# Kernel optimization log

Hardware: AMD Instinct MI355X
Metric: run time of the kernel (lower is better)

The kernel has to match this reference:

```python
import jax, jax.numpy as jnp
import numpy as np

N_NODES = 50000
N_EDGES = 1_600_000
N_REL = 8
D_IN = 128
D_OUT = 128


def _unique_edges(rng, n_nodes, n_rel, n_edges):
    # Torch module clamps the dense adjacency to 0/1, so duplicate
    # (rel, src, dst) triples collapse; generate unique edges so the
    # edge-list formulation matches exactly.
    m = 2 * n_edges
    src = rng.integers(0, n_nodes, m)
    dst = rng.integers(0, n_nodes, m)
    et = rng.integers(0, n_rel, m)
    key = (et.astype(np.int64) * n_nodes + src) * n_nodes + dst
    _, idx = np.unique(key, return_index=True)
    idx = np.sort(idx)[:n_edges]
    return src[idx], dst[idx], et[idx]


def setup_inputs() -> dict:
    key = jax.random.key(0)
    kx, kw, kr, kb = jax.random.split(key, 4)
    rng = np.random.default_rng(0)
    src, dst, et = _unique_edges(rng, N_NODES, N_REL, N_EDGES)
    bound = 1.0 / np.sqrt(D_OUT)
    return {
        "x": jax.random.normal(kx, (N_NODES, D_IN), dtype=jnp.float32),
        "edge_index": jnp.asarray(np.stack([src, dst]), dtype=jnp.int64),
        "edge_type": jnp.asarray(et, dtype=jnp.int64),
        "weight": jax.random.uniform(kw, (N_REL, D_OUT, D_IN), minval=-bound, maxval=bound, dtype=jnp.float32),
        "root": jax.random.uniform(kr, (D_OUT, D_IN), minval=-bound, maxval=bound, dtype=jnp.float32),
        "bias": jax.random.uniform(kb, (D_OUT,), minval=-bound, maxval=bound, dtype=jnp.float32),
    }


def reference(x, edge_index, edge_type, weight, root, bias):
    # Math identical to: adj[l, src, dst] = 1; adj row-normalized (mean);
    # out = sum_r norm_adj_r @ x @ W_r^T + x @ root^T + bias.
    n_rel, d_out, d_in = weight.shape
    n_nodes = x.shape[0]
    src = edge_index[0]
    dst = edge_index[1]
    seg = (edge_type * n_nodes + src).astype(jnp.int32)  # segment per (rel, node)
    num_seg = n_rel * n_nodes
    # sum of neighbor features per (relation, node): [R*N, d_in]
    agg = jax.ops.segment_sum(x[dst], seg, num_segments=num_seg)
    deg = jax.ops.segment_sum(jnp.ones((src.shape[0],), dtype=x.dtype), seg, num_segments=num_seg)
    norm = jnp.where(deg > 0, 1.0 / deg, 0.0)[:, None]  # mean aggr, nan_to_num(0)
    agg = (agg * norm).reshape(n_rel, n_nodes, d_in)
    out = jnp.einsum('rnd,rod->no', agg, weight)
    out = out + x @ root.T + bias[None]
    return out
```

## Files before the change

### kernel.cpp

```cpp
#include <hip/hip_runtime.h>


#define D 128
#define SCAN_CHUNK 2048
#define SEG_BITS 9
#define SEGS_PER_BUCKET 512
#define NBLK 128

typedef __attribute__((ext_vector_type(8))) short short8;
typedef __attribute__((ext_vector_type(4))) float v4f;
typedef __attribute__((ext_vector_type(4))) unsigned uint4v;

#define GLOAD_LDS16(gptr, lptr) \
    __builtin_amdgcn_global_load_lds((const __attribute__((address_space(1))) void*)(gptr), \
                                     (__attribute__((address_space(3))) void*)(lptr), 16, 0, 0)

__device__ __forceinline__ unsigned short f2b(float f) {
    union { float f; unsigned u; } v; v.f = f;
    unsigned r = v.u + 0x7fffu + ((v.u >> 16) & 1u);
    return (unsigned short)(r >> 16);
}
__device__ __forceinline__ float blo(unsigned u) {
    union { unsigned u; float f; } v; v.u = u << 16; return v.f;
}
__device__ __forceinline__ float bhi(unsigned u) {
    union { unsigned u; float f; } v; v.u = u & 0xffff0000u; return v.f;
}

__global__ void cvt_bf16_all(const float* __restrict__ x, long long nx,
                             const float* __restrict__ w, long long nw,
                             const float* __restrict__ root, long long nr,
                             unsigned short* __restrict__ xB,
                             unsigned short* __restrict__ xRow,
                             unsigned short* __restrict__ wB, int nN) {
    long long i = ((long long)blockIdx.x * blockDim.x + threadIdx.x) * 4;
    if (i < nx) {
        float4 v = *(const float4*)(x + i);
        uint2 p;
        p.x = (unsigned)f2b(v.x) | ((unsigned)f2b(v.y) << 16);
        p.y = (unsigned)f2b(v.z) | ((unsigned)f2b(v.w) << 16);
        long long n = i >> 7;
        int d = (int)(i & 127);
        size_t o = (size_t)(d >> 5) * (size_t)nN * 32 + (size_t)n * 32 + (d & 31);
        *(uint2*)(xB + o) = p;
        *(uint2*)(xRow + i) = p;
        return;
    }
    const float* src;
    unsigned short* dst;
    long long j;
    if (i < nx + nw) { src = w; dst = wB; j = i - nx; }
    else if (i < nx + nw + nr) { src = root; dst = wB + nw; j = i - nx - nw; }
    else return;
    float4 v = *(const float4*)(src + j);
    uint2 p;
    p.x = (unsigned)f2b(v.x) | ((unsigned)f2b(v.y) << 16);
    p.y = (unsigned)f2b(v.z) | ((unsigned)f2b(v.w) << 16);
    *(uint2*)(dst + j) = p;
}

__global__ __launch_bounds__(256)
void histA(const int* __restrict__ ei, const int* __restrict__ et,
           int* __restrict__ blockHist, int nE, int nN, int B, int epb) {
    __shared__ int lh[1024];
    const int tid = threadIdx.x;
    for (int b = tid; b < B; b += 256) lh[b] = 0;
    __syncthreads();
    const int base = blockIdx.x * epb;
    const int lim = min(base + epb, nE);
    for (int e = base + tid; e < lim; e += 256) {
        int seg = et[e] * nN + ei[e];
        atomicAdd(&lh[seg >> SEG_BITS], 1);
    }
    __syncthreads();
    for (int b = tid; b < B; b += 256)
        blockHist[b * NBLK + blockIdx.x] = lh[b];
}

__global__ __launch_bounds__(256)
void scan1(const int* __restrict__ in, int* __restrict__ excl,
           int* __restrict__ blockSums, int n) {
    __shared__ int t[256];
    const int tid = threadIdx.x;
    const int base = blockIdx.x * SCAN_CHUNK + tid * 8;
    int v[8];
    int tot = 0;
#pragma unroll
    for (int i = 0; i < 8; i++) {
        v[i] = (base + i < n) ? in[base + i] : 0;
        tot += v[i];
    }
    t[tid] = tot;
    __syncthreads();
    for (int off = 1; off < 256; off <<= 1) {
        int add = (tid >= off) ? t[tid - off] : 0;
        __syncthreads();
        t[tid] += add;
        __syncthreads();
    }
    int run = t[tid] - tot;
#pragma unroll
    for (int i = 0; i < 8; i++) {
        if (base + i < n) excl[base + i] = run;
        run += v[i];
    }
    if (tid == 255) blockSums[blockIdx.x] = t[255];
}

__global__ __launch_bounds__(256)
void scan2(int* __restrict__ blockSums, int nb) {
    __shared__ int t[256];
    const int tid = threadIdx.x;
    int v = (tid < nb) ? blockSums[tid] : 0;
    t[tid] = v;
    __syncthreads();
    for (int off = 1; off < 256; off <<= 1) {
        int add = (tid >= off) ? t[tid - off] : 0;
        __syncthreads();
        t[tid] += add;
        __syncthreads();
    }
    if (tid < nb) blockSums[tid] = t[tid] - v;
}

__global__ __launch_bounds__(256)
void scan3s(int* __restrict__ excl, const int* __restrict__ blockSums, int n) {
    const int base = blockIdx.x * SCAN_CHUNK + threadIdx.x * 8;
    const int bs = blockSums[blockIdx.x];
#pragma unroll
    for (int i = 0; i < 8; i++)
        if (base + i < n) excl[base + i] += bs;
}

__global__ __launch_bounds__(256)
void scatterA(const int* __restrict__ ei, const int* __restrict__ et,
              const int* __restrict__ scanned, unsigned* __restrict__ bucketEdges,
              int nE, int nN, int B, int epb) {
    __shared__ int cur[1024];
    const int tid = threadIdx.x;
    for (int b = tid; b < B; b += 256) cur[b] = scanned[b * NBLK + blockIdx.x];
    __syncthreads();
    const int base = blockIdx.x * epb;
    const int lim = min(base + epb, nE);
    for (int e = base + tid; e < lim; e += 256) {
        int seg = et[e] * nN + ei[e];
        int bkt = seg >> SEG_BITS;
        unsigned pk = ((unsigned)(seg & (SEGS_PER_BUCKET - 1)) << 16) | (unsigned)ei[nE + e];
        int pos = atomicAdd(&cur[bkt], 1);
        bucketEdges[pos] = pk;
    }
}

__global__ __launch_bounds__(256)
void segOff(const unsigned* __restrict__ bucketEdges, const int* __restrict__ scanned,
            int* __restrict__ off, unsigned short* __restrict__ sortedDst,
            int nE, int numSeg, int B) {
    __shared__ int lh[SEGS_PER_BUCKET];
    __shared__ int sc[256];
    __shared__ int lcur[SEGS_PER_BUCKET];
    const int tid = threadIdx.x;
    const int b = blockIdx.x;
    const int eBase = scanned[b * NBLK];
    const int eEnd = (b + 1 < B) ? scanned[(b + 1) * NBLK] : nE;
    const int segBase = b * SEGS_PER_BUCKET;
    const int segLim = min(SEGS_PER_BUCKET, numSeg - segBase);

    lh[2 * tid] = 0; lh[2 * tid + 1] = 0;
    __syncthreads();
    for (int i = eBase + tid; i < eEnd; i += 256)
        atomicAdd(&lh[bucketEdges[i] >> 16], 1);
    __syncthreads();
    int a0 = lh[2 * tid], a1 = lh[2 * tid + 1];
    sc[tid] = a0 + a1;
    __syncthreads();
    for (int o = 1; o < 256; o <<= 1) {
        int add = (tid >= o) ? sc[tid - o] : 0;
        __syncthreads();
        sc[tid] += add;
        __syncthreads();
    }
    int pairBase = sc[tid] - (a0 + a1);
    int g0 = eBase + pairBase;
    int g1 = g0 + a0;
    lcur[2 * tid] = g0;
    lcur[2 * tid + 1] = g1;
    if (2 * tid < segLim)     off[segBase + 2 * tid] = g0;
    if (2 * tid + 1 < segLim) off[segBase + 2 * tid + 1] = g1;
    if (b == B - 1 && tid == 0) off[numSeg] = nE;
    __syncthreads();
    for (int i = eBase + tid; i < eEnd; i += 256) {
        unsigned u = bucketEdges[i];
        int pos = atomicAdd(&lcur[u >> 16], 1);
        sortedDst[pos] = (unsigned short)(u & 0xFFFFu);
    }
}

__global__ __launch_bounds__(256)
void rgcn_gather(const unsigned short* __restrict__ xB,
                 const unsigned short* __restrict__ sortedDst,
                 const int* __restrict__ off,
                 unsigned short* __restrict__ Abuf, int nN, size_t SL) {
    const int tid = threadIdx.x;
    const int lane = tid & 63;
    const int idx4 = lane & 3;
    const int grp = lane >> 2;
    const int wv = tid >> 6;
    const int n = blockIdx.x * 64 + wv * 16 + grp;
    const int r = blockIdx.y;
    const int sl = blockIdx.z;
    const bool valid = (n < nN);
    const int seg = valid ? (r * nN + n) : 0;

    const int start = off[seg];
    int cnt = valid ? (off[seg + 1] - start) : 0;

    int mx = cnt;
    mx = max(mx, __shfl_xor(mx, 4));
    mx = max(mx, __shfl_xor(mx, 8));
    mx = max(mx, __shfl_xor(mx, 16));
    mx = max(mx, __shfl_xor(mx, 32));

    float2 acc2[4];
#pragma unroll
    for (int i = 0; i < 4; i++) acc2[i] = make_float2(0.f, 0.f);

    const unsigned short* xSlab = xB + (size_t)sl * nN * 32 + idx4 * 8;

    for (int b = 0; b < mx; b += 4) {
        int myDst = (b + idx4 < cnt) ? (int)sortedDst[start + b + idx4] : 0;
        uint4v v[4];
#pragma unroll
        for (int j = 0; j < 4; j++) {
            int dst = __shfl(myDst, grp * 4 + j);
            bool act = (b + j < cnt);
            v[j] = act ? *(const uint4v*)(xSlab + ((size_t)dst << 5))
                       : (uint4v){0u, 0u, 0u, 0u};
        }
#pragma unroll
        for (int j = 0; j < 4; j++) {
            acc2[0].x += blo(v[j].x); acc2[0].y += bhi(v[j].x);
            acc2[1].x += blo(v[j].y); acc2[1].y += bhi(v[j].y);
            acc2[2].x += blo(v[j].z); acc2[2].y += bhi(v[j].z);
            acc2[3].x += blo(v[j].w); acc2[3].y += bhi(v[j].w);
        }
    }

    if (valid) {
        float s = cnt > 0 ? 1.0f / (float)cnt : 0.f;
        uint4v pkt;
        pkt.x = (unsigned)f2b(acc2[0].x * s) | ((unsigned)f2b(acc2[0].y * s) << 16);
        pkt.y = (unsigned)f2b(acc2[1].x * s) | ((unsigned)f2b(acc2[1].y * s) << 16);
        pkt.z = (unsigned)f2b(acc2[2].x * s) | ((unsigned)f2b(acc2[2].y * s) << 16);
        pkt.w = (unsigned)f2b(acc2[3].x * s) | ((unsigned)f2b(acc2[3].y * s) << 16);
        __builtin_nontemporal_store(pkt,
            (uint4v*)(Abuf + (size_t)r * SL + (size_t)n * D + sl * 32 + idx4 * 8));
    }
}

__global__ __launch_bounds__(256)
void rgcn_gemm_mfma(const unsigned short* __restrict__ A,
                    const unsigned short* __restrict__ wB,
                    const float* __restrict__ bias,
                    float* __restrict__ out, int nN, int nRel, size_t SL) {
    __shared__ __align__(16) unsigned short As[2][64 * 64];
    __shared__ __align__(16) unsigned short Bs[2][128 * 64];
    const int tid = threadIdx.x;
    const int wave = tid >> 6;
    const int lane = tid & 63;
    const int wm = wave & 1;
    const int wn = wave >> 1;
    const int m16 = lane & 15;
    const int q = lane >> 4;
    const int row0 = blockIdx.x * 64;

    v4f acc[2][4];
#pragma unroll
    for (int i = 0; i < 2; i++)
#pragma unroll
        for (int j = 0; j < 4; j++) acc[i][j] = (v4f){0.f, 0.f, 0.f, 0.f};

    const int sw = m16 & 7;
    int aoff[2][2], boff[4][2];
#pragma unroll
    for (int mt = 0; mt < 2; mt++) {
        int row = wm * 32 + mt * 16 + m16;
#pragma unroll
        for (int kb = 0; kb < 2; kb++)
            aoff[mt][kb] = row * 64 + (((kb * 4 + q) ^ sw) * 8);
    }
#pragma unroll
    for (int nt = 0; nt < 4; nt++) {
        int o = wn * 64 + nt * 16 + m16;
#pragma unroll
        for (int kb = 0; kb < 2; kb++)
            boff[nt][kb] = o * 64 + (((kb * 4 + q) ^ sw) * 8);
    }

    const int l8 = lane >> 3;
    const int gd = (lane & 7) ^ l8;
    const size_t aBase = (size_t)(row0 + wave * 16 + l8) * D + gd * 8;
    const size_t bBase = (size_t)(wave * 32 + l8) * D + gd * 8;

    const int nT = 2 * (nRel + 1);

#define STAGE(buf, t) do { \
        const int s_ = (t) >> 1, h_ = (t) & 1; \
        const unsigned short* ga_ = A + (size_t)s_ * SL + h_ * 64 + aBase; \
        const unsigned short* gb_ = wB + (size_t)s_ * (D * D) + h_ * 64 + bBase; \
        GLOAD_LDS16(ga_,        &As[buf][(wave * 2 + 0) * 512]); \
        GLOAD_LDS16(ga_ + 1024, &As[buf][(wave * 2 + 1) * 512]); \
        GLOAD_LDS16(gb_,        &Bs[buf][(wave * 4 + 0) * 512]); \
        GLOAD_LDS16(gb_ + 1024, &Bs[buf][(wave * 4 + 1) * 512]); \
        GLOAD_LDS16(gb_ + 2048, &Bs[buf][(wave * 4 + 2) * 512]); \
        GLOAD_LDS16(gb_ + 3072, &Bs[buf][(wave * 4 + 3) * 512]); \
    } while (0)

    STAGE(0, 0);
    __syncthreads();
    int cur = 0;
    for (int t = 0; t < nT; ++t) {
        if (t + 1 < nT) STAGE(cur ^ 1, t + 1);
        const unsigned short* Ab = As[cur];
        const unsigned short* Bb = Bs[cur];
        short8 a[2][2], b[4][2];
#pragma unroll
        for (int kb = 0; kb < 2; kb++) {
#pragma unroll
            for (int mt = 0; mt < 2; mt++)
                a[mt][kb] = *(const short8*)&Ab[aoff[mt][kb]];
#pragma unroll
            for (int nt = 0; nt < 4; nt++)
                b[nt][kb] = *(const short8*)&Bb[boff[nt][kb]];
        }
#pragma unroll
        for (int kb = 0; kb < 2; kb++)
#pragma unroll
            for (int mt = 0; mt < 2; mt++)
#pragma unroll
                for (int nt = 0; nt < 4; nt++)
                    acc[mt][nt] = __builtin_amdgcn_mfma_f32_16x16x32_bf16(
                        a[mt][kb], b[nt][kb], acc[mt][nt], 0, 0, 0);
        __syncthreads();
        cur ^= 1;
    }
#undef STAGE

#pragma unroll
    for (int mt = 0; mt < 2; mt++) {
#pragma unroll
        for (int nt = 0; nt < 4; nt++) {
            int col = wn * 64 + nt * 16 + m16;
            float bi = bias[col];
#pragma unroll
            for (int reg = 0; reg < 4; reg++) {
                int rrow = row0 + wm * 32 + mt * 16 + q * 4 + reg;
                if (rrow < nN)
                    out[(size_t)rrow * D + col] = acc[mt][nt][reg] + bi;
            }
        }
    }
}

extern "C" void kernel_launch(void* const* d_in, const int* in_sizes, int n_in,
                              void* d_out, int out_size, void* d_ws, size_t ws_size,
                              hipStream_t stream) {
    const float* x    = (const float*)d_in[0];
    const int*   ei   = (const int*)d_in[1];
    const int*   et   = (const int*)d_in[2];
    const float* w    = (const float*)d_in[3];
    const float* root = (const float*)d_in[4];
    const float* bias = (const float*)d_in[5];
    float* out = (float*)d_out;

    const int nN   = in_sizes[0] / D;
    const int nE   = in_sizes[2];
    const int nRel = in_sizes[3] / (D * D);
    const int numSeg = nRel * nN;
    const int B = (numSeg + SEGS_PER_BUCKET - 1) >> SEG_BITS;
    const int nBH = B * NBLK;
    const int epb = (nE + NBLK - 1) / NBLK;
    const int nNalloc = (nN + 63) & ~63;
    const size_t SL = (size_t)nNalloc * D;

    char* p = (char*)d_ws;
    unsigned* bucketEdges   = (unsigned*)p;        p += (size_t)nE * sizeof(unsigned);
    unsigned short* sortedDst = (unsigned short*)p; p += (size_t)nE * sizeof(unsigned short);
    p = (char*)(((uintptr_t)p + 255) & ~(uintptr_t)255);
    int* off       = (int*)p;  p += (size_t)(numSeg + 1) * sizeof(int);
    int* blockHist = (int*)p;  p += (size_t)nBH * sizeof(int);
    int* scanned   = (int*)p;  p += (size_t)nBH * sizeof(int);
    int* blockSums = (int*)p;  p += 256 * sizeof(int);
    p = (char*)(((uintptr_t)p + 255) & ~(uintptr_t)255);
    unsigned short* xB   = (unsigned short*)p;  p += (size_t)nN * D * sizeof(unsigned short);
    unsigned short* wBc  = (unsigned short*)p;  p += (size_t)(nRel + 1) * D * D * sizeof(unsigned short);
    p = (char*)(((uintptr_t)p + 255) & ~(uintptr_t)255);
    unsigned short* Abuf = (unsigned short*)p;
    unsigned short* xRow = Abuf + (size_t)nRel * SL;

    const int nScanBlocks = (nBH + SCAN_CHUNK - 1) / SCAN_CHUNK;

    histA<<<NBLK, 256, 0, stream>>>(ei, et, blockHist, nE, nN, B, epb);
    scan1<<<nScanBlocks, 256, 0, stream>>>(blockHist, scanned, blockSums, nBH);
    scan2<<<1, 256, 0, stream>>>(blockSums, nScanBlocks);
    scan3s<<<nScanBlocks, 256, 0, stream>>>(scanned, blockSums, nBH);
    scatterA<<<NBLK, 256, 0, stream>>>(ei, et, scanned, bucketEdges, nE, nN, B, epb);
    segOff<<<B, 256, 0, stream>>>(bucketEdges, scanned, off, sortedDst, nE, numSeg, B);

    long long nx = (long long)nN * D;
    long long nw = (long long)nRel * D * D;
    long long nr = (long long)D * D;
    long long ncvt = (nx + nw + nr) / 4;
    cvt_bf16_all<<<(int)((ncvt + 255) / 256), 256, 0, stream>>>(x, nx, w, nw, root, nr,
                                                                xB, xRow, wBc, nN);

    dim3 gg((nN + 63) / 64, nRel, 4);
    rgcn_gather<<<gg, 256, 0, stream>>>(xB, sortedDst, off, Abuf, nN, SL);

    rgcn_gemm_mfma<<<(nN + 63) / 64, 256, 0, stream>>>(Abuf, wBc, bias, out, nN, nRel, SL);
}
```

Measured before the change: 278.4 us.

## Sort segments by degree for balanced gather and fold scan fixup into consumers

Builds a degree histogram in segOff and a permutation of segments grouped by degree (a counting sort), so each gather wavefront processes segments with similar neighbor counts and loses less time to divergence from the per-wave max loop. It also removes the scan3s kernel by adding blockSums when scatterA and segOff read offsets, and uses packed f32 adds in the accumulation. The cost is an extra permBuild kernel, a perm indirection, and scattered output writes in the gather.

```diff
diff --git a/kernel.cpp b/kernel.cpp
--- a/kernel.cpp
+++ b/kernel.cpp
@@ -6,9 +6,11 @@
 #define SEG_BITS 9
 #define SEGS_PER_BUCKET 512
 #define NBLK 128
+#define NDEG 32
 
 typedef __attribute__((ext_vector_type(8))) short short8;
 typedef __attribute__((ext_vector_type(4))) float v4f;
+typedef __attribute__((ext_vector_type(2))) float f32x2;
 typedef __attribute__((ext_vector_type(4))) unsigned uint4v;
 
 #define GLOAD_LDS16(gptr, lptr) \
@@ -79,7 +81,12 @@
 
 __global__ __launch_bounds__(256)
 void scan1(const int* __restrict__ in, int* __restrict__ excl,
-           int* __restrict__ blockSums, int n) {
+           int* __restrict__ blockSums, int* __restrict__ degHist,
+           int* __restrict__ cursor32, int n) {
+    if (blockIdx.x == 0 && threadIdx.x < 2 * NDEG) {
+        if (threadIdx.x < NDEG) degHist[threadIdx.x] = 0;
+        else cursor32[threadIdx.x - NDEG] = 0;
+    }
     __shared__ int t[256];
     const int tid = threadIdx.x;
     const int base = blockIdx.x * SCAN_CHUNK + tid * 8;
@@ -124,21 +131,16 @@
 }
 
 __global__ __launch_bounds__(256)
-void scan3s(int* __restrict__ excl, const int* __restrict__ blockSums, int n) {
-    const int base = blockIdx.x * SCAN_CHUNK + threadIdx.x * 8;
-    const int bs = blockSums[blockIdx.x];
-#pragma unroll
-    for (int i = 0; i < 8; i++)
-        if (base + i < n) excl[base + i] += bs;
-}
-
-__global__ __launch_bounds__(256)
 void scatterA(const int* __restrict__ ei, const int* __restrict__ et,
-              const int* __restrict__ scanned, unsigned* __restrict__ bucketEdges,
+              const int* __restrict__ scanned, const int* __restrict__ blockSums,
+              unsigned* __restrict__ bucketEdges,
               int nE, int nN, int B, int epb) {
     __shared__ int cur[1024];
     const int tid = threadIdx.x;
-    for (int b = tid; b < B; b += 256) cur[b] = scanned[b * NBLK + blockIdx.x];
+    for (int b = tid; b < B; b += 256) {
+        int idx = b * NBLK + blockIdx.x;
+        cur[b] = scanned[idx] + blockSums[idx >> 11];
+    }
     __syncthreads();
     const int base = blockIdx.x * epb;
     const int lim = min(base + epb, nE);
@@ -153,24 +155,34 @@
 
 __global__ __launch_bounds__(256)
 void segOff(const unsigned* __restrict__ bucketEdges, const int* __restrict__ scanned,
+            const int* __restrict__ blockSums,
             int* __restrict__ off, unsigned short* __restrict__ sortedDst,
-            int nE, int numSeg, int B) {
+            int* __restrict__ degHist, int nE, int numSeg, int B) {
     __shared__ int lh[SEGS_PER_BUCKET];
     __shared__ int sc[256];
     __shared__ int lcur[SEGS_PER_BUCKET];
+    __shared__ int dh[NDEG];
     const int tid = threadIdx.x;
     const int b = blockIdx.x;
-    const int eBase = scanned[b * NBLK];
-    const int eEnd = (b + 1 < B) ? scanned[(b + 1) * NBLK] : nE;
+    const int i0 = b * NBLK;
+    const int eBase = scanned[i0] + blockSums[i0 >> 11];
+    int eEnd = nE;
+    if (b + 1 < B) {
+        const int i1 = (b + 1) * NBLK;
+        eEnd = scanned[i1] + blockSums[i1 >> 11];
+    }
     const int segBase = b * SEGS_PER_BUCKET;
     const int segLim = min(SEGS_PER_BUCKET, numSeg - segBase);
 
     lh[2 * tid] = 0; lh[2 * tid + 1] = 0;
+    if (tid < NDEG) dh[tid] = 0;
     __syncthreads();
     for (int i = eBase + tid; i < eEnd; i += 256)
         atomicAdd(&lh[bucketEdges[i] >> 16], 1);
     __syncthreads();
     int a0 = lh[2 * tid], a1 = lh[2 * tid + 1];
+    if (2 * tid < segLim)     atomicAdd(&dh[min(a0, NDEG - 1)], 1);
+    if (2 * tid + 1 < segLim) atomicAdd(&dh[min(a1, NDEG - 1)], 1);
     sc[tid] = a0 + a1;
     __syncthreads();
     for (int o = 1; o < 256; o <<= 1) {
@@ -193,23 +205,59 @@
         int pos = atomicAdd(&lcur[u >> 16], 1);
         sortedDst[pos] = (unsigned short)(u & 0xFFFFu);
     }
+    __syncthreads();
+    if (tid < NDEG && dh[tid]) atomicAdd(&degHist[tid], dh[tid]);
+}
+
+__global__ __launch_bounds__(256)
+void permBuild(const int* __restrict__ off, const int* __restrict__ degHist,
+               int* __restrict__ cursor32, int* __restrict__ perm, int numSeg) {
+    __shared__ int lcnt[NDEG];
+    __shared__ int lbase[NDEG];
+    __shared__ int gbase[NDEG];
+    const int tid = threadIdx.x;
+    if (tid < NDEG) lcnt[tid] = 0;
+    __syncthreads();
+    int s[4], bkt[4], lpos[4];
+#pragma unroll
+    for (int i = 0; i < 4; i++) {
+        s[i] = blockIdx.x * 1024 + i * 256 + tid;
+        bkt[i] = -1;
+        if (s[i] < numSeg) {
+            int c = off[s[i] + 1] - off[s[i]];
+            bkt[i] = min(c, NDEG - 1);
+            lpos[i] = atomicAdd(&lcnt[bkt[i]], 1);
+        }
+    }
+    __syncthreads();
+    if (tid < NDEG) {
+        lbase[tid] = lcnt[tid] ? atomicAdd(&cursor32[tid], lcnt[tid]) : 0;
+        int run = 0;
+        for (int k = 0; k < tid; k++) run += degHist[k];
+        gbase[tid] = run;
+    }
+    __syncthreads();
+#pragma unroll
+    for (int i = 0; i < 4; i++)
+        if (bkt[i] >= 0)
+            perm[gbase[bkt[i]] + lbase[bkt[i]] + lpos[i]] = s[i];
 }
 
 __global__ __launch_bounds__(256)
 void rgcn_gather(const unsigned short* __restrict__ xB,
                  const unsigned short* __restrict__ sortedDst,
-                 const int* __restrict__ off,
-                 unsigned short* __restrict__ Abuf, int nN, size_t SL) {
+                 const int* __restrict__ off, const int* __restrict__ perm,
+                 unsigned short* __restrict__ Abuf, int nN, int numSeg,
+                 size_t SL, unsigned long long M) {
     const int tid = threadIdx.x;
     const int lane = tid & 63;
     const int idx4 = lane & 3;
     const int grp = lane >> 2;
     const int wv = tid >> 6;
-    const int n = blockIdx.x * 64 + wv * 16 + grp;
-    const int r = blockIdx.y;
-    const int sl = blockIdx.z;
-    const bool valid = (n < nN);
-    const int seg = valid ? (r * nN + n) : 0;
+    const int gsi = blockIdx.x * 64 + wv * 16 + grp;
+    const int sl = blockIdx.y;
+    const bool valid = (gsi < numSeg);
+    const int seg = valid ? perm[gsi] : 0;
 
     const int start = off[seg];
     int cnt = valid ? (off[seg + 1] - start) : 0;
@@ -220,9 +268,9 @@
     mx = max(mx, __shfl_xor(mx, 16));
     mx = max(mx, __shfl_xor(mx, 32));
 
-    float2 acc2[4];
-#pragma unroll
-    for (int i = 0; i < 4; i++) acc2[i] = make_float2(0.f, 0.f);
+    f32x2 acc2[4];
+#pragma unroll
+    for (int i = 0; i < 4; i++) acc2[i] = (f32x2){0.f, 0.f};
 
     const unsigned short* xSlab = xB + (size_t)sl * nN * 32 + idx4 * 8;
 
@@ -238,14 +286,20 @@
         }
 #pragma unroll
         for (int j = 0; j < 4; j++) {
-            acc2[0].x += blo(v[j].x); acc2[0].y += bhi(v[j].x);
-            acc2[1].x += blo(v[j].y); acc2[1].y += bhi(v[j].y);
-            acc2[2].x += blo(v[j].z); acc2[2].y += bhi(v[j].z);
-            acc2[3].x += blo(v[j].w); acc2[3].y += bhi(v[j].w);
+            f32x2 t0 = (f32x2){blo(v[j].x), bhi(v[j].x)};
+            f32x2 t1 = (f32x2){blo(v[j].y), bhi(v[j].y)};
+            f32x2 t2 = (f32x2){blo(v[j].z), bhi(v[j].z)};
+            f32x2 t3 = (f32x2){blo(v[j].w), bhi(v[j].w)};
+            asm("v_pk_add_f32 %0, %0, %1" : "+v"(acc2[0]) : "v"(t0));
+            asm("v_pk_add_f32 %0, %0, %1" : "+v"(acc2[1]) : "v"(t1));
+            asm("v_pk_add_f32 %0, %0, %1" : "+v"(acc2[2]) : "v"(t2));
+            asm("v_pk_add_f32 %0, %0, %1" : "+v"(acc2[3]) : "v"(t3));
         }
     }
 
     if (valid) {
+        const int r = (int)(((unsigned long long)seg * M) >> 48);
+        const int n = seg - r * nN;
         float s = cnt > 0 ? 1.0f / (float)cnt : 0.f;
         uint4v pkt;
         pkt.x = (unsigned)f2b(acc2[0].x * s) | ((unsigned)f2b(acc2[0].y * s) << 16);
@@ -381,6 +435,7 @@
     const int epb = (nE + NBLK - 1) / NBLK;
     const int nNalloc = (nN + 63) & ~63;
     const size_t SL = (size_t)nNalloc * D;
+    const unsigned long long M = ((1ULL << 48) + nN - 1) / nN;
 
     char* p = (char*)d_ws;
     unsigned* bucketEdges   = (unsigned*)p;        p += (size_t)nE * sizeof(unsigned);
@@ -390,6 +445,10 @@
     int* blockHist = (int*)p;  p += (size_t)nBH * sizeof(int);
     int* scanned   = (int*)p;  p += (size_t)nBH * sizeof(int);
     int* blockSums = (int*)p;  p += 256 * sizeof(int);
+    int* degHist   = (int*)p;  p += NDEG * sizeof(int);
+    int* cursor32  = (int*)p;  p += NDEG * sizeof(int);
+    p = (char*)(((uintptr_t)p + 255) & ~(uintptr_t)255);
+    int* perm      = (int*)p;  p += (size_t)numSeg * sizeof(int);
     p = (char*)(((uintptr_t)p + 255) & ~(uintptr_t)255);
     unsigned short* xB   = (unsigned short*)p;  p += (size_t)nN * D * sizeof(unsigned short);
     unsigned short* wBc  = (unsigned short*)p;  p += (size_t)(nRel + 1) * D * D * sizeof(unsigned short);
@@ -400,11 +459,12 @@
     const int nScanBlocks = (nBH + SCAN_CHUNK - 1) / SCAN_CHUNK;
 
     histA<<<NBLK, 256, 0, stream>>>(ei, et, blockHist, nE, nN, B, epb);
-    scan1<<<nScanBlocks, 256, 0, stream>>>(blockHist, scanned, blockSums, nBH);
+    scan1<<<nScanBlocks, 256, 0, stream>>>(blockHist, scanned, blockSums, degHist, cursor32, nBH);
     scan2<<<1, 256, 0, stream>>>(blockSums, nScanBlocks);
-    scan3s<<<nScanBlocks, 256, 0, stream>>>(scanned, blockSums, nBH);
-    scatterA<<<NBLK, 256, 0, stream>>>(ei, et, scanned, bucketEdges, nE, nN, B, epb);
-    segOff<<<B, 256, 0, stream>>>(bucketEdges, scanned, off, sortedDst, nE, numSeg, B);
+    scatterA<<<NBLK, 256, 0, stream>>>(ei, et, scanned, blockSums, bucketEdges, nE, nN, B, epb);
+    segOff<<<B, 256, 0, stream>>>(bucketEdges, scanned, blockSums, off, sortedDst, degHist,
+                                  nE, numSeg, B);
+    permBuild<<<(numSeg + 1023) / 1024, 256, 0, stream>>>(off, degHist, cursor32, perm, numSeg);
 
     long long nx = (long long)nN * D;
     long long nw = (long long)nRel * D * D;
@@ -413,8 +473,8 @@
     cvt_bf16_all<<<(int)((ncvt + 255) / 256), 256, 0, stream>>>(x, nx, w, nw, root, nr,
                                                                 xB, xRow, wBc, nN);
 
-    dim3 gg((nN + 63) / 64, nRel, 4);
-    rgcn_gather<<<gg, 256, 0, stream>>>(xB, sortedDst, off, Abuf, nN, SL);
+    dim3 gg((numSeg + 63) / 64, 4);
+    rgcn_gather<<<gg, 256, 0, stream>>>(xB, sortedDst, off, perm, Abuf, nN, numSeg, SL, M);
 
     rgcn_gemm_mfma<<<(nN + 63) / 64, 256, 0, stream>>>(Abuf, wBc, bias, out, nN, nRel, SL);
 }
```

Measured after the change: 302.3 us. 1.09x slower.
